# Optimization experiments

Measured on AMD Instinct MI355X. Metric: run time of the kernel, lower is better.

## Reference

```python
import jax, jax.numpy as jnp
import numpy as np

F = 845   # feature_num
P = 39    # field_num
K = 32    # implicit_vector_dim
B = 32768 # batch


def _field_ids():
    # feature_to_field(n) = n if n < 13 else (n - 13) // K + 13
    n = np.arange(F)
    return np.where(n < 13, n, (n - 13) // K + 13).astype(np.int32)


def setup_inputs() -> dict:
    key = jax.random.key(0)
    k0, k1, k2, k3 = jax.random.split(key, 4)
    # scale inputs/params down so the quadratic term does not saturate sigmoid
    X = jax.random.normal(k0, (B, F), jnp.float32) * 0.05
    field_matrix = jax.random.normal(k1, (F, P, K), jnp.float32) * 0.1
    a = jax.random.normal(k2, (F, F), jnp.float32)
    w_lin = jax.random.normal(k3, (F, 1), jnp.float32) * 0.02
    b_lin = jnp.zeros((1,), jnp.float32)
    return {"X": X, "field_matrix": field_matrix, "a": a,
            "w_lin": w_lin, "b_lin": b_lin}


def reference(X, field_matrix, a, w_lin, b_lin):
    # The original loop computes, per feature i:
    #   result[b] += X[b, i] * sum_j a[i, j] * X[b, j]
    #                * <field_matrix[i, field(i)], field_matrix[j, field(j)]>
    # i.e. a batched quadratic form X W X^T (diagonal) with
    #   W[i, j] = a[i, j] * (V @ V.T)[i, j],  V[i] = field_matrix[i, field(i)].
    fid = jnp.asarray(_field_ids())
    V = field_matrix[jnp.arange(F), fid]        # [F, K] own-field vectors
    W = a * (V @ V.T)                           # [F, F]
    quad = jnp.sum((X @ W) * X, axis=-1)        # [B]
    lin = X @ w_lin[:, 0] + b_lin[0]            # [B]
    # original casts to double at the end; we stay in float32 (math identical)
    return jax.nn.sigmoid(lin + quad)
```

## Files before the change

kernel.cpp:

```cpp
#include <hip/hip_runtime.h>
#include <hip/hip_bf16.h>
#include <math.h>

typedef unsigned short ushort_t;
typedef unsigned int   uint_t;

typedef __attribute__((ext_vector_type(8))) __bf16 bf16x8;
typedef __attribute__((ext_vector_type(4))) float  f32x4;

#define BATCH 32768
#define FDIM  845
#define FP    896
#define NBLK  7
#define MBLK  256

#define PREP_BLKS 196
#define CONV_BLKS 27040
#define PAD_BLKS  8192

__device__ __forceinline__ int fld(int n) { return (n < 13) ? n : (((n - 13) >> 5) + 13); }

__device__ __forceinline__ ushort_t f2bf(float f) {
    uint_t u = __builtin_bit_cast(uint_t, f);
    uint_t r = u + 0x7FFFu + ((u >> 16) & 1u);
    return (ushort_t)(r >> 16);
}
__device__ __forceinline__ float bf2f(ushort_t h) {
    uint_t u = ((uint_t)h) << 16;
    return __builtin_bit_cast(float, u);
}

__device__ __forceinline__ void gload_lds16(const ushort_t* g, ushort_t* l) {
    __builtin_amdgcn_global_load_lds(
        (const __attribute__((address_space(1))) void*)g,
        (__attribute__((address_space(3))) void*)l, 16, 0, 0);
}

__global__ __launch_bounds__(256, 2)
void prep_all(const float* __restrict__ X, const float* __restrict__ fm,
              const float* __restrict__ a, const float* __restrict__ wl,
              ushort_t* __restrict__ Xb, ushort_t* __restrict__ WbT) {
    __shared__ float    As[64 * 65];
    __shared__ float    At[64 * 65];
    __shared__ ushort_t Vi[64 * 32];
    __shared__ ushort_t Vj[64 * 32];

    const int tid = threadIdx.x;
    const int bx  = blockIdx.x;

    if (bx >= PREP_BLKS) {
        const int cb = bx - PREP_BLKS;
        if (cb < CONV_BLKS) {
            const uint_t e0 = ((uint_t)cb * 256 + tid) * 4;
            const float4 x = *(const float4*)(X + e0);
            const uint_t row0 = e0 / 845u;
            const uint_t col0 = e0 - row0 * 845u;
            const float xv[4] = {x.x, x.y, x.z, x.w};
            #pragma unroll
            for (int j = 0; j < 4; ++j) {
                const uint_t row = row0 + ((col0 + j >= 845u) ? 1u : 0u);
                Xb[(size_t)(e0 + j) + 51u * row] = f2bf(xv[j]);
            }
        } else {
            const uint_t p   = (uint_t)(cb - CONV_BLKS) * 256 + tid;
            const uint_t row = p >> 6, q = p & 63;
            if (q < 51) Xb[(size_t)row * FP + FDIM + q] = (q == 0) ? (ushort_t)0x3F80 : (ushort_t)0;
        }
        return;
    }

    const int i0 = (bx % 14) * 64, j0 = (bx / 14) * 64;
    const int ib128 = i0 >> 7, jb128 = j0 >> 7;
    if (ib128 > jb128) return;
    const bool offd = (ib128 < jb128);
    const int wave = tid >> 6, lane = tid & 63;
    const int l15  = lane & 15, l4 = lane >> 4;

    {
        const int row = tid >> 2;
        const int kq  = (tid & 3) * 8;
        union { ushort_t u[8]; uint4 v; } pi, pj;
        const int gi = i0 + row, gj = j0 + row;
        #pragma unroll
        for (int q = 0; q < 8; ++q) {
            float vi = 0.0f, vj = 0.0f;
            if (gi < FDIM) vi = fm[(size_t)(gi * 39 + fld(gi)) * 32 + kq + q];
            if (gj < FDIM) vj = fm[(size_t)(gj * 39 + fld(gj)) * 32 + kq + q];
            pi.u[q] = f2bf(vi);
            pj.u[q] = f2bf(vj);
        }
        *(uint4*)&Vi[row * 32 + kq] = pi.v;
        *(uint4*)&Vj[row * 32 + kq] = pj.v;
    }
    {
        const int row = tid >> 2, seg = tid & 3;
        const int gi  = i0 + row, gj2 = j0 + row;
        #pragma unroll
        for (int q = 0; q < 16; ++q) {
            const int cl = seg * 16 + q;
            const int gj = j0 + cl;
            As[row * 65 + cl] = (gi < FDIM && gj < FDIM) ? a[(size_t)gi * FDIM + gj] : 0.0f;
            if (offd) {
                const int gi2 = i0 + cl;
                At[row * 65 + cl] = (gj2 < FDIM && gi2 < FDIM) ? a[(size_t)gj2 * FDIM + gi2] : 0.0f;
            }
        }
    }
    __syncthreads();

    bf16x8 af = *(const bf16x8*)&Vj[(wave * 16 + l15) * 32 + l4 * 8];
    f32x4 acc[4];
    #pragma unroll
    for (int it = 0; it < 4; ++it) {
        bf16x8 bf = *(const bf16x8*)&Vi[(it * 16 + l15) * 32 + l4 * 8];
        acc[it] = __builtin_amdgcn_mfma_f32_16x16x32_bf16(af, bf, (f32x4){0.f,0.f,0.f,0.f}, 0, 0, 0);
    }

    #pragma unroll
    for (int it = 0; it < 4; ++it) {
        #pragma unroll
        for (int r = 0; r < 4; ++r) {
            const int jl = wave * 16 + l4 * 4 + r;
            const int il = it * 16 + l15;
            const int gi = i0 + il, gj = j0 + jl;
            float aij = As[il * 65 + jl];
            if (offd) aij += At[jl * 65 + il];
            float w = acc[it][r] * aij;
            if (gj == FDIM) w = (gi < FDIM) ? wl[gi] : 0.0f;
            WbT[(size_t)gj * FP + gi] = f2bf(w);
        }
    }
}

__global__ __launch_bounds__(256, 2)
void ffm_gemm(const ushort_t* __restrict__ Xb, const ushort_t* __restrict__ WbT,
              float* __restrict__ qpart) {
    __shared__ ushort_t As[128 * 64];
    __shared__ ushort_t Bs[128 * 64];

    const int tid  = threadIdx.x;
    const int wave = tid >> 6, lane = tid & 63;
    const int l15  = lane & 15, l4 = lane >> 4;
    const int wm   = wave >> 1, wn = wave & 1;

    const int bid  = blockIdx.x;
    const int xcd  = bid & 7;
    const int slot = bid >> 3;
    const int nb   = slot % 7;
    const int m0   = (xcd * 32 + slot / 7) * 128;
    const int n0   = nb * 128;

    const int r8 = lane >> 3;
    const int s8 = lane & 7;

    f32x4 acc[4][4];
    #pragma unroll
    for (int i = 0; i < 4; ++i)
        #pragma unroll
        for (int j = 0; j < 4; ++j) acc[i][j] = (f32x4){0.f, 0.f, 0.f, 0.f};

    const int kimax = (nb + 1) * 2;
    for (int kt = 0; kt < kimax; ++kt) {
        const int k0 = kt * 64;
        __syncthreads();
        #pragma unroll
        for (int h = 0; h < 4; ++h) {
            const int row = wave * 32 + h * 8 + r8;
            const int sg  = s8 ^ (row & 7);
            gload_lds16(Xb  + (size_t)(m0 + row) * FP + k0 + sg * 8,
                        &As[(wave * 32 + h * 8) * 64]);
            gload_lds16(WbT + (size_t)(n0 + row) * FP + k0 + sg * 8,
                        &Bs[(wave * 32 + h * 8) * 64]);
        }
        __syncthreads();

        bf16x8 af[4][2], bfv[4][2];
        #pragma unroll
        for (int i = 0; i < 4; ++i) {
            const int r = wm * 64 + i * 16 + l15;
            #pragma unroll
            for (int h = 0; h < 2; ++h) {
                const int s = (h * 4 + l4) ^ (r & 7);
                af[i][h] = *(const bf16x8*)&As[r * 64 + s * 8];
            }
        }
        #pragma unroll
        for (int j = 0; j < 4; ++j) {
            const int r = wn * 64 + j * 16 + l15;
            #pragma unroll
            for (int h = 0; h < 2; ++h) {
                const int s = (h * 4 + l4) ^ (r & 7);
                bfv[j][h] = *(const bf16x8*)&Bs[r * 64 + s * 8];
            }
        }
        #pragma unroll
        for (int i = 0; i < 4; ++i)
            #pragma unroll
            for (int j = 0; j < 4; ++j) {
                acc[i][j] = __builtin_amdgcn_mfma_f32_16x16x32_bf16(af[i][0], bfv[j][0], acc[i][j], 0, 0, 0);
                acc[i][j] = __builtin_amdgcn_mfma_f32_16x16x32_bf16(af[i][1], bfv[j][1], acc[i][j], 0, 0, 0);
            }
    }

    float q[4][4] = {};
    #pragma unroll
    for (int i = 0; i < 4; ++i)
        #pragma unroll
        for (int j = 0; j < 4; ++j) {
            const int col = n0 + wn * 64 + j * 16 + l15;
            #pragma unroll
            for (int r = 0; r < 4; ++r) {
                const int row = m0 + wm * 64 + i * 16 + l4 * 4 + r;
                q[i][r] += acc[i][j][r] * bf2f(Xb[(size_t)row * FP + col]);
            }
        }
    #pragma unroll
    for (int off = 1; off < 16; off <<= 1)
        #pragma unroll
        for (int i = 0; i < 4; ++i)
            #pragma unroll
            for (int r = 0; r < 4; ++r) q[i][r] += __shfl_xor(q[i][r], off, 64);

    if (l15 == 0) {
        float* dst = qpart + (size_t)(nb * 2 + wn) * BATCH;
        #pragma unroll
        for (int i = 0; i < 4; ++i)
            #pragma unroll
            for (int r = 0; r < 4; ++r)
                dst[m0 + wm * 64 + i * 16 + l4 * 4 + r] = q[i][r];
    }
}

__global__ void finish(const float* __restrict__ qpart, const float* __restrict__ blin,
                       float* __restrict__ out) {
    int b = blockIdx.x * 256 + threadIdx.x;
    float s = blin[0];
    #pragma unroll
    for (int p = 0; p < 14; ++p) s += qpart[(size_t)p * BATCH + b];
    out[b] = 1.0f / (1.0f + expf(-s));
}

extern "C" void kernel_launch(void* const* d_in, const int* in_sizes, int n_in,
                              void* d_out, int out_size, void* d_ws, size_t ws_size,
                              hipStream_t stream) {
    const float* X  = (const float*)d_in[0];
    const float* fm = (const float*)d_in[1];
    const float* a  = (const float*)d_in[2];
    const float* wl = (const float*)d_in[3];
    const float* bl = (const float*)d_in[4];
    float* out = (float*)d_out;

    char* ws = (char*)d_ws;
    ushort_t* Xb    = (ushort_t*)ws;
    ushort_t* WbT   = (ushort_t*)(ws + 58720256);
    float*    qpart = (float*)   (ws + 60383232);

    prep_all<<<PREP_BLKS + CONV_BLKS + PAD_BLKS, 256, 0, stream>>>(X, fm, a, wl, Xb, WbT);
    ffm_gemm<<<MBLK * NBLK,        256, 0, stream>>>(Xb, WbT, qpart);
    finish  <<<BATCH / 256,        256, 0, stream>>>(qpart, bl, out);
}
```

Measured before the change: 222.7 us.

## Load W operand straight from global into registers and reduce partials in LDS

The GEMM kernel no longer stages the W tile in shared memory. Each wave reads its B fragments directly from global memory (likely L2-resident) into registers, which halves LDS usage and could allow higher occupancy. The block order is reversed so the longest upper-triangular column blocks launch first. The two column-half partial sums are combined through LDS before being written, so the finish kernel reads 7 partial arrays instead of 14. The cost is uncoalesced per-lane global loads for B, whose latency is no longer hidden behind LDS staging.

```diff
diff --git a/kernel.cpp b/kernel.cpp
--- a/kernel.cpp
+++ b/kernel.cpp
@@ -136,7 +136,6 @@
 void ffm_gemm(const ushort_t* __restrict__ Xb, const ushort_t* __restrict__ WbT,
               float* __restrict__ qpart) {
     __shared__ ushort_t As[128 * 64];
-    __shared__ ushort_t Bs[128 * 64];
 
     const int tid  = threadIdx.x;
     const int wave = tid >> 6, lane = tid & 63;
@@ -146,7 +145,7 @@
     const int bid  = blockIdx.x;
     const int xcd  = bid & 7;
     const int slot = bid >> 3;
-    const int nb   = slot % 7;
+    const int nb   = 6 - (slot % 7);
     const int m0   = (xcd * 32 + slot / 7) * 128;
     const int n0   = nb * 128;
 
@@ -158,6 +157,8 @@
     for (int i = 0; i < 4; ++i)
         #pragma unroll
         for (int j = 0; j < 4; ++j) acc[i][j] = (f32x4){0.f, 0.f, 0.f, 0.f};
+
+    const ushort_t* bbase = WbT + (size_t)(n0 + wn * 64 + l15) * FP + l4 * 8;
 
     const int kimax = (nb + 1) * 2;
     for (int kt = 0; kt < kimax; ++kt) {
@@ -167,39 +168,33 @@
         for (int h = 0; h < 4; ++h) {
             const int row = wave * 32 + h * 8 + r8;
             const int sg  = s8 ^ (row & 7);
-            gload_lds16(Xb  + (size_t)(m0 + row) * FP + k0 + sg * 8,
+            gload_lds16(Xb + (size_t)(m0 + row) * FP + k0 + sg * 8,
                         &As[(wave * 32 + h * 8) * 64]);
-            gload_lds16(WbT + (size_t)(n0 + row) * FP + k0 + sg * 8,
-                        &Bs[(wave * 32 + h * 8) * 64]);
-        }
+        }
+        bf16x8 bfv[4][2];
+        #pragma unroll
+        for (int j = 0; j < 4; ++j)
+            #pragma unroll
+            for (int h = 0; h < 2; ++h)
+                bfv[j][h] = *(const bf16x8*)(bbase + (size_t)(j * 16) * FP + k0 + h * 32);
         __syncthreads();
 
-        bf16x8 af[4][2], bfv[4][2];
         #pragma unroll
         for (int i = 0; i < 4; ++i) {
             const int r = wm * 64 + i * 16 + l15;
-            #pragma unroll
-            for (int h = 0; h < 2; ++h) {
-                const int s = (h * 4 + l4) ^ (r & 7);
-                af[i][h] = *(const bf16x8*)&As[r * 64 + s * 8];
-            }
-        }
-        #pragma unroll
-        for (int j = 0; j < 4; ++j) {
-            const int r = wn * 64 + j * 16 + l15;
-            #pragma unroll
-            for (int h = 0; h < 2; ++h) {
-                const int s = (h * 4 + l4) ^ (r & 7);
-                bfv[j][h] = *(const bf16x8*)&Bs[r * 64 + s * 8];
-            }
-        }
-        #pragma unroll
-        for (int i = 0; i < 4; ++i)
+            bf16x8 af0, af1;
+            {
+                const int s0 = l4 ^ (r & 7);
+                const int s1 = (4 + l4) ^ (r & 7);
+                af0 = *(const bf16x8*)&As[r * 64 + s0 * 8];
+                af1 = *(const bf16x8*)&As[r * 64 + s1 * 8];
+            }
             #pragma unroll
             for (int j = 0; j < 4; ++j) {
-                acc[i][j] = __builtin_amdgcn_mfma_f32_16x16x32_bf16(af[i][0], bfv[j][0], acc[i][j], 0, 0, 0);
-                acc[i][j] = __builtin_amdgcn_mfma_f32_16x16x32_bf16(af[i][1], bfv[j][1], acc[i][j], 0, 0, 0);
-            }
+                acc[i][j] = __builtin_amdgcn_mfma_f32_16x16x32_bf16(af0, bfv[j][0], acc[i][j], 0, 0, 0);
+                acc[i][j] = __builtin_amdgcn_mfma_f32_16x16x32_bf16(af1, bfv[j][1], acc[i][j], 0, 0, 0);
+            }
+        }
     }
 
     float q[4][4] = {};
@@ -221,13 +216,25 @@
             #pragma unroll
             for (int r = 0; r < 4; ++r) q[i][r] += __shfl_xor(q[i][r], off, 64);
 
-    if (l15 == 0) {
-        float* dst = qpart + (size_t)(nb * 2 + wn) * BATCH;
+    __syncthreads();
+    float* buf = (float*)As;
+    if (wn == 1 && l15 == 0) {
         #pragma unroll
         for (int i = 0; i < 4; ++i)
             #pragma unroll
             for (int r = 0; r < 4; ++r)
-                dst[m0 + wm * 64 + i * 16 + l4 * 4 + r] = q[i][r];
+                buf[wm * 64 + i * 16 + l4 * 4 + r] = q[i][r];
+    }
+    __syncthreads();
+    if (wn == 0 && l15 == 0) {
+        float* dst = qpart + (size_t)nb * BATCH;
+        #pragma unroll
+        for (int i = 0; i < 4; ++i)
+            #pragma unroll
+            for (int r = 0; r < 4; ++r) {
+                const int rl = wm * 64 + i * 16 + l4 * 4 + r;
+                dst[m0 + rl] = q[i][r] + buf[rl];
+            }
     }
 }
 
@@ -236,7 +243,7 @@
     int b = blockIdx.x * 256 + threadIdx.x;
     float s = blin[0];
     #pragma unroll
-    for (int p = 0; p < 14; ++p) s += qpart[(size_t)p * BATCH + b];
+    for (int p = 0; p < 7; ++p) s += qpart[(size_t)p * BATCH + b];
     out[b] = 1.0f / (1.0f + expf(-s));
 }
 
@@ -253,7 +260,7 @@
     char* ws = (char*)d_ws;
     ushort_t* Xb    = (ushort_t*)ws;
     ushort_t* WbT   = (ushort_t*)(ws + 58720256);
-    float*    qpart = (float*)   (ws + 60383232);
+    float*    qpart = (float*)   (ws + 60325888);
 
     prep_all<<<PREP_BLKS + CONV_BLKS + PAD_BLKS, 256, 0, stream>>>(X, fm, a, wl, Xb, WbT);
     ffm_gemm<<<MBLK * NBLK,        256, 0, stream>>>(Xb, WbT, qpart);
```

New measurement: 264.6 us. 1.19x slower.

## Enlarge GEMM tile to 256x128 with each wave owning full N width

Applied to the files above, without the earlier changes.

The quadratic-form GEMM now uses 256-row M tiles, with each of the four waves computing a 64x128 sub-tile, in place of a 2x2 wave grid of 64x64. This halves the block count and the number of partial-sum columns written to qpart and read by the finish kernel, and it raises per-wave B-fragment reuse. The N-block order is reversed so the longest triangular K loops are scheduled first. In exchange, the accumulator count doubles, which raises register pressure and may lower occupancy under the two-blocks-per-SM launch bound. Shared memory per block also grows.

```diff
diff --git a/kernel.cpp b/kernel.cpp
--- a/kernel.cpp
+++ b/kernel.cpp
@@ -12,7 +12,7 @@
 #define FDIM  845
 #define FP    896
 #define NBLK  7
-#define MBLK  256
+#define MSTR  128
 
 #define PREP_BLKS 196
 #define CONV_BLKS 27040
@@ -135,49 +135,53 @@
 __global__ __launch_bounds__(256, 2)
 void ffm_gemm(const ushort_t* __restrict__ Xb, const ushort_t* __restrict__ WbT,
               float* __restrict__ qpart) {
-    __shared__ ushort_t As[128 * 64];
+    __shared__ ushort_t As[256 * 64];
     __shared__ ushort_t Bs[128 * 64];
 
     const int tid  = threadIdx.x;
     const int wave = tid >> 6, lane = tid & 63;
     const int l15  = lane & 15, l4 = lane >> 4;
-    const int wm   = wave >> 1, wn = wave & 1;
 
     const int bid  = blockIdx.x;
     const int xcd  = bid & 7;
     const int slot = bid >> 3;
-    const int nb   = slot % 7;
-    const int m0   = (xcd * 32 + slot / 7) * 128;
+    const int nb   = 6 - (slot % 7);
+    const int m0   = (xcd * 16 + slot / 7) * 256;
     const int n0   = nb * 128;
 
     const int r8 = lane >> 3;
     const int s8 = lane & 7;
 
-    f32x4 acc[4][4];
+    f32x4 acc[4][8];
     #pragma unroll
     for (int i = 0; i < 4; ++i)
         #pragma unroll
-        for (int j = 0; j < 4; ++j) acc[i][j] = (f32x4){0.f, 0.f, 0.f, 0.f};
+        for (int j = 0; j < 8; ++j) acc[i][j] = (f32x4){0.f, 0.f, 0.f, 0.f};
 
     const int kimax = (nb + 1) * 2;
     for (int kt = 0; kt < kimax; ++kt) {
         const int k0 = kt * 64;
         __syncthreads();
         #pragma unroll
+        for (int h = 0; h < 8; ++h) {
+            const int row = wave * 64 + h * 8 + r8;
+            const int sg  = s8 ^ (row & 7);
+            gload_lds16(Xb + (size_t)(m0 + row) * FP + k0 + sg * 8,
+                        &As[(wave * 64 + h * 8) * 64]);
+        }
+        #pragma unroll
         for (int h = 0; h < 4; ++h) {
             const int row = wave * 32 + h * 8 + r8;
             const int sg  = s8 ^ (row & 7);
-            gload_lds16(Xb  + (size_t)(m0 + row) * FP + k0 + sg * 8,
-                        &As[(wave * 32 + h * 8) * 64]);
             gload_lds16(WbT + (size_t)(n0 + row) * FP + k0 + sg * 8,
                         &Bs[(wave * 32 + h * 8) * 64]);
         }
         __syncthreads();
 
-        bf16x8 af[4][2], bfv[4][2];
+        bf16x8 af[4][2];
         #pragma unroll
         for (int i = 0; i < 4; ++i) {
-            const int r = wm * 64 + i * 16 + l15;
+            const int r = wave * 64 + i * 16 + l15;
             #pragma unroll
             for (int h = 0; h < 2; ++h) {
                 const int s = (h * 4 + l4) ^ (r & 7);
@@ -185,49 +189,46 @@
             }
         }
         #pragma unroll
-        for (int j = 0; j < 4; ++j) {
-            const int r = wn * 64 + j * 16 + l15;
-            #pragma unroll
-            for (int h = 0; h < 2; ++h) {
-                const int s = (h * 4 + l4) ^ (r & 7);
-                bfv[j][h] = *(const bf16x8*)&Bs[r * 64 + s * 8];
-            }
-        }
+        for (int j = 0; j < 8; ++j) {
+            const int r = j * 16 + l15;
+            const int s0 = l4 ^ (r & 7);
+            const int s1 = (4 + l4) ^ (r & 7);
+            const bf16x8 b0 = *(const bf16x8*)&Bs[r * 64 + s0 * 8];
+            const bf16x8 b1 = *(const bf16x8*)&Bs[r * 64 + s1 * 8];
+            #pragma unroll
+            for (int i = 0; i < 4; ++i) {
+                acc[i][j] = __builtin_amdgcn_mfma_f32_16x16x32_bf16(af[i][0], b0, acc[i][j], 0, 0, 0);
+                acc[i][j] = __builtin_amdgcn_mfma_f32_16x16x32_bf16(af[i][1], b1, acc[i][j], 0, 0, 0);
+            }
+        }
+    }
+
+    float q[4][4] = {};
+    #pragma unroll
+    for (int i = 0; i < 4; ++i)
+        #pragma unroll
+        for (int j = 0; j < 8; ++j) {
+            const int col = n0 + j * 16 + l15;
+            #pragma unroll
+            for (int r = 0; r < 4; ++r) {
+                const int row = m0 + wave * 64 + i * 16 + l4 * 4 + r;
+                q[i][r] += acc[i][j][r] * bf2f(Xb[(size_t)row * FP + col]);
+            }
+        }
+    #pragma unroll
+    for (int off = 1; off < 16; off <<= 1)
         #pragma unroll
         for (int i = 0; i < 4; ++i)
             #pragma unroll
-            for (int j = 0; j < 4; ++j) {
-                acc[i][j] = __builtin_amdgcn_mfma_f32_16x16x32_bf16(af[i][0], bfv[j][0], acc[i][j], 0, 0, 0);
-                acc[i][j] = __builtin_amdgcn_mfma_f32_16x16x32_bf16(af[i][1], bfv[j][1], acc[i][j], 0, 0, 0);
-            }
-    }
-
-    float q[4][4] = {};
-    #pragma unroll
-    for (int i = 0; i < 4; ++i)
-        #pragma unroll
-        for (int j = 0; j < 4; ++j) {
-            const int col = n0 + wn * 64 + j * 16 + l15;
-            #pragma unroll
-            for (int r = 0; r < 4; ++r) {
-                const int row = m0 + wm * 64 + i * 16 + l4 * 4 + r;
-                q[i][r] += acc[i][j][r] * bf2f(Xb[(size_t)row * FP + col]);
-            }
-        }
-    #pragma unroll
-    for (int off = 1; off < 16; off <<= 1)
+            for (int r = 0; r < 4; ++r) q[i][r] += __shfl_xor(q[i][r], off, 64);
+
+    if (l15 == 0) {
+        float* dst = qpart + (size_t)nb * BATCH;
         #pragma unroll
         for (int i = 0; i < 4; ++i)
             #pragma unroll
-            for (int r = 0; r < 4; ++r) q[i][r] += __shfl_xor(q[i][r], off, 64);
-
-    if (l15 == 0) {
-        float* dst = qpart + (size_t)(nb * 2 + wn) * BATCH;
-        #pragma unroll
-        for (int i = 0; i < 4; ++i)
-            #pragma unroll
             for (int r = 0; r < 4; ++r)
-                dst[m0 + wm * 64 + i * 16 + l4 * 4 + r] = q[i][r];
+                dst[m0 + wave * 64 + i * 16 + l4 * 4 + r] = q[i][r];
     }
 }
 
@@ -236,7 +237,7 @@
     int b = blockIdx.x * 256 + threadIdx.x;
     float s = blin[0];
     #pragma unroll
-    for (int p = 0; p < 14; ++p) s += qpart[(size_t)p * BATCH + b];
+    for (int p = 0; p < 7; ++p) s += qpart[(size_t)p * BATCH + b];
     out[b] = 1.0f / (1.0f + expf(-s));
 }
 
@@ -253,9 +254,9 @@
     char* ws = (char*)d_ws;
     ushort_t* Xb    = (ushort_t*)ws;
     ushort_t* WbT   = (ushort_t*)(ws + 58720256);
-    float*    qpart = (float*)   (ws + 60383232);
+    float*    qpart = (float*)   (ws + 60325888);
 
     prep_all<<<PREP_BLKS + CONV_BLKS + PAD_BLKS, 256, 0, stream>>>(X, fm, a, wl, Xb, WbT);
-    ffm_gemm<<<MBLK * NBLK,        256, 0, stream>>>(Xb, WbT, qpart);
+    ffm_gemm<<<MSTR * NBLK,        256, 0, stream>>>(Xb, WbT, qpart);
     finish  <<<BATCH / 256,        256, 0, stream>>>(qpart, bl, out);
 }
```

After: 228.0 us. 1.02x slower.
